# Kernel tuning notes

Hardware: AMD Instinct MI355X
Metric: run time of the kernel (lower is better)

The kernel has to match this reference:

```python
import jax, jax.numpy as jnp
import numpy as np

N_NODES, N_EDGES, N_GRAPHS = 65536, 131072, 2048
F_NODE, F_EDGE, DIM, DIM1, DIM2 = 78, 10, 256, 512, 256
FP_DIM, FP2, FP3, NCB = 1489, 128, 256, 2

PNAMES = []
for _l in (1, 2, 3):
    PNAMES += [f"e{_l}w", f"e{_l}b", f"n{_l}w1", f"n{_l}b1", f"n{_l}w2", f"n{_l}b2",
               f"bn{_l}g", f"bn{_l}b", f"bn{_l}m", f"bn{_l}v"]
PNAMES += ["fcg_w", "fcg_b", "fp1_w", "fp1_b", "fp2_w", "fp2_b",
           "fb1_w", "fb1_b", "fb2_w", "fb2_b", "fb3_w", "fb3_b", "fb4_w", "fb4_b"]


def _params(key):
    ks = iter(jax.random.split(key, 64))
    def rn(*s):
        return jax.random.normal(next(ks), s, dtype=jnp.float32) * 0.05
    def ru(*s):
        return jax.random.uniform(next(ks), s, dtype=jnp.float32)
    p = {}
    for l, ci in zip((1, 2, 3), (F_NODE, DIM1, DIM1)):
        h = DIM if l == 1 else DIM1
        p[f"e{l}w"] = rn(ci, F_EDGE); p[f"e{l}b"] = rn(ci)          # GINEConv edge lin: 10 -> in_channels
        p[f"n{l}w1"] = rn(h, ci);     p[f"n{l}b1"] = rn(h)
        p[f"n{l}w2"] = rn(DIM1, h);   p[f"n{l}b2"] = rn(DIM1)
        p[f"bn{l}g"] = ru(DIM1) + 0.5; p[f"bn{l}b"] = rn(DIM1)
        p[f"bn{l}m"] = rn(DIM1);       p[f"bn{l}v"] = ru(DIM1) + 0.5
    p["fcg_w"] = rn(DIM2, DIM1);  p["fcg_b"] = rn(DIM2)
    p["fp1_w"] = rn(FP2, FP_DIM); p["fp1_b"] = rn(FP2)
    p["fp2_w"] = rn(FP3, FP2);    p["fp2_b"] = rn(FP3)
    for i, (o, ci) in enumerate([(256, 512), (128, 256), (64, 128), (NCB, 64)], 1):
        p[f"fb{i}_w"] = rn(o, ci); p[f"fb{i}_b"] = rn(o)
    return p


def setup_inputs() -> dict:
    key = jax.random.key(0)
    k = jax.random.split(key, 6)
    inp = {
        "x": jax.random.normal(k[0], (N_NODES, F_NODE), dtype=jnp.float32),
        "finger": jax.random.uniform(k[1], (N_GRAPHS, FP_DIM), dtype=jnp.float32),
        "edge_attr": jax.random.normal(k[2], (N_EDGES, F_EDGE), dtype=jnp.float32),
        "edge_index": jax.random.randint(k[3], (2, N_EDGES), 0, N_NODES),
        "batch": jnp.sort(jax.random.randint(k[4], (N_NODES,), 0, N_GRAPHS)),
    }
    inp.update(_params(k[5]))
    return inp


def _lin(x, w, b):
    return x @ w.T + b


def _bn(x, g, b, m, v):
    # eval-mode BatchNorm1d with running stats
    return (x - m) * jax.lax.rsqrt(v + 1e-5) * g + b


def _forward(x, finger, edge_attr, edge_index, batch, p):
    src, dst = edge_index[0], edge_index[1]
    h = x
    for l in (1, 2, 3):
        # GINEConv (eps=0): out = nn(x + sum_j relu(x_j + lin(edge_attr)))
        e = _lin(edge_attr, p[f"e{l}w"], p[f"e{l}b"])               # [E, Cin]
        m = jax.nn.relu(h[src] + e)                                   # gather + edge add
        agg = jax.ops.segment_sum(m, dst, num_segments=N_NODES)      # scatter-add
        t = h + agg
        t = _lin(jax.nn.relu(_lin(t, p[f"n{l}w1"], p[f"n{l}b1"])), p[f"n{l}w2"], p[f"n{l}b2"])
        h = _bn(jax.nn.relu(t), p[f"bn{l}g"], p[f"bn{l}b"], p[f"bn{l}m"], p[f"bn{l}v"])
    g = jax.ops.segment_sum(h, batch, num_segments=N_GRAPHS)         # global_add_pool
    g = jax.nn.relu(_lin(g, p["fcg_w"], p["fcg_b"]))                 # fc_1 (dropout is eval no-op)
    fp = jax.nn.relu(_lin(finger, p["fp1_w"], p["fp1_b"]))
    fp = jax.nn.relu(_lin(fp, p["fp2_w"], p["fp2_b"]))
    y = jnp.concatenate([g, fp], axis=1)                              # [B, 512]
    for i in (1, 2, 3):
        y = jax.nn.relu(_lin(y, p[f"fb{i}_w"], p[f"fb{i}_b"]))
    y = _lin(y, p["fb4_w"], p["fb4_b"])
    return jax.nn.sigmoid(y)


def reference(x, finger, edge_attr, edge_index, batch,
              e1w, e1b, n1w1, n1b1, n1w2, n1b2, bn1g, bn1b, bn1m, bn1v,
              e2w, e2b, n2w1, n2b1, n2w2, n2b2, bn2g, bn2b, bn2m, bn2v,
              e3w, e3b, n3w1, n3b1, n3w2, n3b2, bn3g, bn3b, bn3m, bn3v,
              fcg_w, fcg_b, fp1_w, fp1_b, fp2_w, fp2_b,
              fb1_w, fb1_b, fb2_w, fb2_b, fb3_w, fb3_b, fb4_w, fb4_b):
    args = dict(locals())
    p = {k: args[k] for k in PNAMES}
    return _forward(x, finger, edge_attr, edge_index, batch, p)
```

## Files before the change

### kernel.cpp

```cpp
#include <hip/hip_runtime.h>
#include <stdint.h>

typedef unsigned short u16;
typedef unsigned int u32;
typedef __bf16 bf16x8 __attribute__((ext_vector_type(8)));
typedef float f32x4 __attribute__((ext_vector_type(4)));

#define N_NODES 65536
#define N_EDGES 131072
#define N_GRAPHS 2048

static __device__ __forceinline__ float bf2f(u16 u) {
  union { u32 u; float f; } v; v.u = ((u32)u) << 16; return v.f;
}
static __device__ __forceinline__ u16 f2bf(float f) {
  union { float f; u32 u; } v; v.f = f;
  u32 r = v.u + 0x7fffu + ((v.u >> 16) & 1u);
  return (u16)(r >> 16);
}
static __device__ __forceinline__ void gl16(const void* g, void* l) {
  __builtin_amdgcn_global_load_lds(
      (__attribute__((address_space(1))) void*)(g),
      (__attribute__((address_space(3))) void*)(l), 16, 0, 0);
}

template <int EPI>
__global__ __launch_bounds__(256) void gemm_bt64(
    const u16* __restrict__ A, const u16* __restrict__ W,
    const float* __restrict__ bias, const float* __restrict__ scale,
    const float* __restrict__ shift, u16* __restrict__ Cp,
    int K, int ldc) {
  __shared__ u16 As[128 * 64];
  __shared__ u16 Bs[128 * 64];
  const u32 gx = gridDim.x;
  const u32 nwg = gx * gridDim.y;
  u32 lid = blockIdx.y * gx + blockIdx.x;
  if ((nwg & 7u) == 0u) {
    const u32 cpx = nwg >> 3;
    lid = (lid & 7u) * cpx + (lid >> 3);
  }
  const int bm = (int)(lid / gx) * 128;
  const int bn = (int)(lid % gx) * 128;
  const int tid = threadIdx.x;
  const int lane = tid & 63;
  const int wid = tid >> 6;
  const int wr = wid >> 1, wc = wid & 1;
  const int lg = lane >> 4, lr = lane & 15;

  f32x4 acc[4][4];
#pragma unroll
  for (int i = 0; i < 4; ++i)
#pragma unroll
    for (int j = 0; j < 4; ++j) acc[i][j] = (f32x4){0.f, 0.f, 0.f, 0.f};

  const int srow8 = tid >> 3;
  const int gslot = ((tid & 7) ^ (srow8 & 7)) * 8;
  const u16* Ag[4];
  const u16* Wg[4];
#pragma unroll
  for (int p = 0; p < 4; ++p) {
    Ag[p] = A + (size_t)(bm + p * 32 + srow8) * K + gslot;
    Wg[p] = W + (size_t)(bn + p * 32 + srow8) * K + gslot;
  }
  u16* dA = &As[tid * 8];
  u16* dB = &Bs[tid * 8];

  for (int k0 = 0; k0 < K; k0 += 64) {
#pragma unroll
    for (int p = 0; p < 4; ++p) {
      gl16(Ag[p] + k0, dA + p * 2048);
      gl16(Wg[p] + k0, dB + p * 2048);
    }
    __syncthreads();
#pragma unroll
    for (int kk = 0; kk < 2; ++kk) {
      const int slot = ((kk * 4 + lg) ^ (lr & 7)) * 8;
      bf16x8 af[4], bfv[4];
#pragma unroll
      for (int i = 0; i < 4; ++i)
        af[i] = *(const bf16x8*)&As[(wr * 64 + i * 16 + lr) * 64 + slot];
#pragma unroll
      for (int j = 0; j < 4; ++j)
        bfv[j] = *(const bf16x8*)&Bs[(wc * 64 + j * 16 + lr) * 64 + slot];
#pragma unroll
      for (int i = 0; i < 4; ++i)
#pragma unroll
        for (int j = 0; j < 4; ++j)
          acc[i][j] = __builtin_amdgcn_mfma_f32_16x16x32_bf16(
              af[i], bfv[j], acc[i][j], 0, 0, 0);
    }
    __syncthreads();
  }

#pragma unroll
  for (int i = 0; i < 4; ++i) {
#pragma unroll
    for (int j = 0; j < 4; ++j) {
#pragma unroll
      for (int r = 0; r < 4; ++r) {
        const int grow = bm + wr * 64 + i * 16 + lg * 4 + r;
        const int gcol = bn + wc * 64 + j * 16 + lr;
        float v = acc[i][j][r] + bias[gcol];
        v = fmaxf(v, 0.f);
        if (EPI == 1) v = v * scale[gcol] + shift[gcol];
        Cp[(size_t)grow * ldc + gcol] = f2bf(v);
      }
    }
  }
}

template <int EPI>
__global__ __launch_bounds__(256) void gemm_bt(
    const u16* __restrict__ A, const u16* __restrict__ W,
    const float* __restrict__ bias, const float* __restrict__ scale,
    const float* __restrict__ shift, u16* __restrict__ Cp,
    int K, int ldc, int coff) {
  __shared__ u16 As[128 * 32];
  __shared__ u16 Bs[128 * 32];
  const u32 gx = gridDim.x;
  const u32 nwg = gx * gridDim.y;
  u32 lid = blockIdx.y * gx + blockIdx.x;
  if ((nwg & 7u) == 0u) {
    const u32 cpx = nwg >> 3;
    lid = (lid & 7u) * cpx + (lid >> 3);
  }
  const int bm = (int)(lid / gx) * 128;
  const int bn = (int)(lid % gx) * 128;
  const int tid = threadIdx.x;
  const int lane = tid & 63;
  const int wid = tid >> 6;
  const int wr = wid >> 1, wc = wid & 1;
  const int lg = lane >> 4, lr = lane & 15;

  f32x4 acc[4][4];
#pragma unroll
  for (int i = 0; i < 4; ++i)
#pragma unroll
    for (int j = 0; j < 4; ++j) acc[i][j] = (f32x4){0.f, 0.f, 0.f, 0.f};

  const int srow = tid >> 2;
  const int c8 = (tid & 3) * 8;
  const u16* Ag0 = A + (size_t)(bm + srow) * K + c8;
  const u16* Ag1 = A + (size_t)(bm + 64 + srow) * K + c8;
  const u16* Wg0 = W + (size_t)(bn + srow) * K + c8;
  const u16* Wg1 = W + (size_t)(bn + 64 + srow) * K + c8;
  u16* lA0 = &As[tid * 8];
  u16* lA1 = &As[2048 + tid * 8];
  u16* lB0 = &Bs[tid * 8];
  u16* lB1 = &Bs[2048 + tid * 8];

  for (int k0 = 0; k0 < K; k0 += 32) {
    gl16(Ag0 + k0, lA0);
    gl16(Ag1 + k0, lA1);
    gl16(Wg0 + k0, lB0);
    gl16(Wg1 + k0, lB1);
    __syncthreads();
    bf16x8 af[4], bfv[4];
#pragma unroll
    for (int i = 0; i < 4; ++i)
      af[i] = *(const bf16x8*)&As[(wr * 64 + i * 16 + lr) * 32 + lg * 8];
#pragma unroll
    for (int j = 0; j < 4; ++j)
      bfv[j] = *(const bf16x8*)&Bs[(wc * 64 + j * 16 + lr) * 32 + lg * 8];
#pragma unroll
    for (int i = 0; i < 4; ++i)
#pragma unroll
      for (int j = 0; j < 4; ++j)
        acc[i][j] = __builtin_amdgcn_mfma_f32_16x16x32_bf16(af[i], bfv[j],
                                                            acc[i][j], 0, 0, 0);
    __syncthreads();
  }

#pragma unroll
  for (int i = 0; i < 4; ++i) {
#pragma unroll
    for (int j = 0; j < 4; ++j) {
#pragma unroll
      for (int r = 0; r < 4; ++r) {
        const int grow = bm + wr * 64 + i * 16 + lg * 4 + r;
        const int gcol = bn + wc * 64 + j * 16 + lr;
        float v = acc[i][j][r] + bias[gcol];
        v = fmaxf(v, 0.f);
        if (EPI == 1) v = v * scale[gcol] + shift[gcol];
        Cp[(size_t)grow * ldc + coff + gcol] = f2bf(v);
      }
    }
  }
}

__global__ void hist_deg(const int* __restrict__ dst, int* __restrict__ deg) {
  int e = blockIdx.x * blockDim.x + threadIdx.x;
  if (e < N_EDGES) atomicAdd(&deg[dst[e]], 1);
}

__global__ __launch_bounds__(1024) void scan_rowptr(const int* __restrict__ deg,
                                                    int* __restrict__ rowptr) {
  __shared__ int lds[1024];
  const int t = threadIdx.x;
  const int base = t * 64;
  int s = 0;
  for (int i = 0; i < 64; ++i) s += deg[base + i];
  lds[t] = s;
  __syncthreads();
  for (int ofs = 1; ofs < 1024; ofs <<= 1) {
    int v = (t >= ofs) ? lds[t - ofs] : 0;
    __syncthreads();
    lds[t] += v;
    __syncthreads();
  }
  int run = (t == 0) ? 0 : lds[t - 1];
  for (int i = 0; i < 64; ++i) {
    rowptr[base + i] = run;
    run += deg[base + i];
  }
  if (t == 1023) rowptr[65536] = run;
}

__global__ void scatter_csr(const int* __restrict__ dst,
                            const int* __restrict__ rowptr,
                            int* __restrict__ deg, int* __restrict__ csr) {
  int e = blockIdx.x * blockDim.x + threadIdx.x;
  if (e >= N_EDGES) return;
  int d = dst[e];
  int pos = atomicSub(&deg[d], 1) - 1;
  csr[rowptr[d] + pos] = e;
}

__global__ __launch_bounds__(128) void gather512(
    const int* __restrict__ rowptr, const int* __restrict__ csr,
    const int* __restrict__ esrc, const float* __restrict__ ea,
    const float* __restrict__ ew, const float* __restrict__ eb,
    const u16* __restrict__ H, u16* __restrict__ T) {
  const int t = threadIdx.x;
  const int c4 = t * 4;
  float w[4][10];
#pragma unroll
  for (int j = 0; j < 4; ++j)
#pragma unroll
    for (int k = 0; k < 10; ++k) w[j][k] = ew[(c4 + j) * 10 + k];
  float eb4[4];
#pragma unroll
  for (int j = 0; j < 4; ++j) eb4[j] = eb[c4 + j];

  const int dend = blockIdx.x * 8 + 8;
  for (int d = blockIdx.x * 8; d < dend; ++d) {
    uint2 hv = *(const uint2*)&H[(size_t)d * 512 + c4];
    float a0 = bf2f((u16)(hv.x & 0xffffu)), a1 = bf2f((u16)(hv.x >> 16));
    float a2 = bf2f((u16)(hv.y & 0xffffu)), a3 = bf2f((u16)(hv.y >> 16));
    const int i1 = rowptr[d + 1];
    for (int i = rowptr[d]; i < i1; ++i) {
      const int eid = csr[i];
      const int s = esrc[eid];
      const float2* eap = (const float2*)(ea + (size_t)eid * 10);
      float2 p0 = eap[0], p1 = eap[1], p2 = eap[2], p3 = eap[3], p4 = eap[4];
      const float ev[10] = {p0.x, p0.y, p1.x, p1.y, p2.x,
                            p2.y, p3.x, p3.y, p4.x, p4.y};
      uint2 hs = *(const uint2*)&H[(size_t)s * 512 + c4];
      float h0 = bf2f((u16)(hs.x & 0xffffu)), h1 = bf2f((u16)(hs.x >> 16));
      float h2 = bf2f((u16)(hs.y & 0xffffu)), h3 = bf2f((u16)(hs.y >> 16));
      float e0 = eb4[0], e1 = eb4[1], e2 = eb4[2], e3 = eb4[3];
#pragma unroll
      for (int k = 0; k < 10; ++k) {
        e0 += ev[k] * w[0][k];
        e1 += ev[k] * w[1][k];
        e2 += ev[k] * w[2][k];
        e3 += ev[k] * w[3][k];
      }
      a0 += fmaxf(h0 + e0, 0.f);
      a1 += fmaxf(h1 + e1, 0.f);
      a2 += fmaxf(h2 + e2, 0.f);
      a3 += fmaxf(h3 + e3, 0.f);
    }
    uint2 r;
    r.x = (u32)f2bf(a0) | ((u32)f2bf(a1) << 16);
    r.y = (u32)f2bf(a2) | ((u32)f2bf(a3) << 16);
    *(uint2*)&T[(size_t)d * 512 + c4] = r;
  }
}

__global__ __launch_bounds__(128) void gather78(
    const int* __restrict__ rowptr, const int* __restrict__ csr,
    const int* __restrict__ esrc, const float* __restrict__ ea,
    const float* __restrict__ ew, const float* __restrict__ eb,
    const float* __restrict__ X, u16* __restrict__ T) {
  const int t = threadIdx.x;
  const bool act = t < 78;
  float w[10];
  float ebv = 0.f;
  if (act) {
#pragma unroll
    for (int k = 0; k < 10; ++k) w[k] = ew[t * 10 + k];
    ebv = eb[t];
  }
  const int dend = blockIdx.x * 8 + 8;
  for (int d = blockIdx.x * 8; d < dend; ++d) {
    float acc = act ? X[(size_t)d * 78 + t] : 0.f;
    const int i1 = rowptr[d + 1];
    for (int i = rowptr[d]; i < i1; ++i) {
      const int eid = csr[i];
      const int s = esrc[eid];
      const float2* eap = (const float2*)(ea + (size_t)eid * 10);
      float2 p0 = eap[0], p1 = eap[1], p2 = eap[2], p3 = eap[3], p4 = eap[4];
      const float ev[10] = {p0.x, p0.y, p1.x, p1.y, p2.x,
                            p2.y, p3.x, p3.y, p4.x, p4.y};
      if (act) {
        float el = ebv;
#pragma unroll
        for (int k = 0; k < 10; ++k) el += ev[k] * w[k];
        acc += fmaxf(X[(size_t)s * 78 + t] + el, 0.f);
      }
    }
    if (t < 96) T[(size_t)d * 96 + t] = act ? f2bf(acc) : (u16)0;
  }
}

struct CvtJob { const float* in; u16* out; int cin; int cout; };
struct CvtJobs { CvtJob j[11]; int blk_ofs[12]; };

__global__ __launch_bounds__(256) void cvt_multi(CvtJobs jb, int njobs) {
  int b = blockIdx.x;
  int ji = 0;
  while (ji + 1 < njobs && b >= jb.blk_ofs[ji + 1]) ++ji;
  const CvtJob J = jb.j[ji];
  int idx = (b - jb.blk_ofs[ji]) * 256 + threadIdx.x;
  int r = idx / J.cout, c = idx - r * J.cout;
  int tot_blocks = jb.blk_ofs[ji + 1] - jb.blk_ofs[ji];
  if (idx >= tot_blocks * 256) return;
  if (idx >= ((tot_blocks * 256) / J.cout) * J.cout && c >= J.cout) return;
  J.out[idx] = (c < J.cin) ? f2bf(J.in[(size_t)r * J.cin + c]) : (u16)0;
}

struct BnJobs { const float* g[3]; const float* b[3]; const float* m[3];
                const float* v[3]; };
__global__ void bn_affine3(BnJobs p, float* __restrict__ bnS) {
  int i = blockIdx.x * blockDim.x + threadIdx.x;
  int l = i >> 9, c = i & 511;
  float s = p.g[l][c] * rsqrtf(p.v[l][c] + 1e-5f);
  bnS[l * 1024 + c] = s;
  bnS[l * 1024 + 512 + c] = p.b[l][c] - p.m[l][c] * s;
}

__global__ void seg_starts(const int* __restrict__ batch, int* __restrict__ start,
                           int n, int ngraphs) {
  int i = blockIdx.x * blockDim.x + threadIdx.x;
  if (i >= n) return;
  int b = batch[i];
  int prev = (i == 0) ? -1 : batch[i - 1];
  for (int g = prev + 1; g <= b; ++g) start[g] = i;
  if (i == n - 1)
    for (int g = b + 1; g <= ngraphs; ++g) start[g] = n;
}

__global__ void cvt_pad(const float* __restrict__ in, u16* __restrict__ out,
                        int rows, int cin, int cout) {
  int idx = blockIdx.x * blockDim.x + threadIdx.x;
  if (idx >= rows * cout) return;
  int rrow = idx / cout, j = idx - rrow * cout;
  out[idx] = (j < cin) ? f2bf(in[(size_t)rrow * cin + j]) : (u16)0;
}

__global__ void pool_sum(const u16* __restrict__ H, const int* __restrict__ start,
                         u16* __restrict__ g) {
  int gi = blockIdx.x, c = threadIdx.x;
  int s = start[gi], e = start[gi + 1];
  float acc = 0.f;
  for (int i = s; i < e; ++i) acc += bf2f(H[(size_t)i * 512 + c]);
  g[gi * 512 + c] = f2bf(acc);
}

__global__ void fb34(const u16* __restrict__ y2, const float* __restrict__ w3,
                     const float* __restrict__ b3, const float* __restrict__ w4,
                     const float* __restrict__ b4, float* __restrict__ out) {
  __shared__ float yr[128];
  __shared__ float h3[64];
  const int row = blockIdx.x, t = threadIdx.x;
  yr[t] = bf2f(y2[row * 128 + t]);
  yr[t + 64] = bf2f(y2[row * 128 + 64 + t]);
  __syncthreads();
  float s = b3[t];
  const float* w3r = &w3[t * 128];
#pragma unroll 8
  for (int k = 0; k < 128; ++k) s += yr[k] * w3r[k];
  h3[t] = fmaxf(s, 0.f);
  __syncthreads();
  if (t < 2) {
    float s4 = b4[t];
    const float* w4r = &w4[t * 64];
    for (int k = 0; k < 64; ++k) s4 += h3[k] * w4r[k];
    out[row * 2 + t] = 1.f / (1.f + expf(-s4));
  }
}

#define CDIV(a, b) (((a) + (b)-1) / (b))

extern "C" void kernel_launch(void* const* d_in, const int* in_sizes, int n_in,
                              void* d_out, int out_size, void* d_ws, size_t ws_size,
                              hipStream_t stream) {
  const float* x = (const float*)d_in[0];
  const float* finger = (const float*)d_in[1];
  const float* ea = (const float*)d_in[2];
  const int* eidx = (const int*)d_in[3];
  const int* batch = (const int*)d_in[4];
  const int* esrc = eidx;
  const int* edst = eidx + N_EDGES;

  const float* P[49];
  for (int i = 5; i < 49; ++i) P[i] = (const float*)d_in[i];
  const float* fcg_w = P[35]; const float* fcg_b = P[36];
  const float* fp1_w = P[37]; const float* fp1_b = P[38];
  const float* fp2_w = P[39]; const float* fp2_b = P[40];
  const float* fb1_w = P[41]; const float* fb1_b = P[42];
  const float* fb2_w = P[43]; const float* fb2_b = P[44];
  const float* fb3_w = P[45]; const float* fb3_b = P[46];
  const float* fb4_w = P[47]; const float* fb4_b = P[48];

  size_t off = 0;
  char* base = (char*)d_ws;
  auto alloc = [&](size_t bytes) -> void* {
    void* p = base + off;
    off = (off + bytes + 255) & ~(size_t)255;
    return p;
  };
  char* BA = (char*)alloc((size_t)N_NODES * 512 * 2);
  char* BB = (char*)alloc((size_t)N_NODES * 512 * 2);
  u16* w11 = (u16*)alloc(256 * 96 * 2);
  u16* w12 = (u16*)alloc(512 * 256 * 2);
  u16* w21 = (u16*)alloc(512 * 512 * 2);
  u16* w22 = (u16*)alloc(512 * 512 * 2);
  u16* w31 = (u16*)alloc(512 * 512 * 2);
  u16* w32 = (u16*)alloc(512 * 512 * 2);
  u16* wfcg = (u16*)alloc(256 * 512 * 2);
  u16* wfp1 = (u16*)alloc(128 * 1504 * 2);
  u16* wfp2 = (u16*)alloc(256 * 128 * 2);
  u16* wfb1 = (u16*)alloc(256 * 512 * 2);
  u16* wfb2 = (u16*)alloc(128 * 256 * 2);
  float* bnS = (float*)alloc(6 * 512 * 4);
  int* start = (int*)alloc(2049 * 4);
  int* deg = (int*)alloc(65536 * 4);
  int* rowptr = (int*)alloc(65537 * 4);
  int* csr = (int*)alloc(131072 * 4);
  if (off > ws_size) return;

  u16* fingb = (u16*)BA;
  u16* gbuf = (u16*)(BA + 6160384);
  u16* y0 = (u16*)(BA + 8257536);
  u16* fpa = (u16*)(BA + 10354688);
  u16* y1 = (u16*)(BA + 10878976);
  u16* y2 = (u16*)(BA + 11927552);

  {
    CvtJobs jb;
    const float* ins[11] = {P[5 + 2], P[5 + 4], P[15 + 2], P[15 + 4], P[25 + 2],
                            P[25 + 4], fcg_w, fp1_w, fp2_w, fb1_w, fb2_w};
    u16* outs[11] = {w11, w12, w21, w22, w31, w32, wfcg, wfp1, wfp2, wfb1, wfb2};
    int rows[11] = {256, 512, 512, 512, 512, 512, 256, 128, 256, 256, 128};
    int cins[11] = {78, 256, 512, 512, 512, 512, 512, 1489, 128, 512, 256};
    int couts[11] = {96, 256, 512, 512, 512, 512, 512, 1504, 128, 512, 256};
    int acc = 0;
    for (int i = 0; i < 11; ++i) {
      jb.j[i].in = ins[i]; jb.j[i].out = outs[i];
      jb.j[i].cin = cins[i]; jb.j[i].cout = couts[i];
      jb.blk_ofs[i] = acc;
      acc += CDIV(rows[i] * couts[i], 256);
    }
    jb.blk_ofs[11] = acc;
    cvt_multi<<<acc, 256, 0, stream>>>(jb, 11);
  }
  {
    BnJobs bj;
    for (int l = 0; l < 3; ++l) {
      int pb = 5 + 10 * l;
      bj.g[l] = P[pb + 6]; bj.b[l] = P[pb + 7];
      bj.m[l] = P[pb + 8]; bj.v[l] = P[pb + 9];
    }
    bn_affine3<<<6, 256, 0, stream>>>(bj, bnS);
  }
  seg_starts<<<CDIV(N_NODES, 256), 256, 0, stream>>>(batch, start, N_NODES, N_GRAPHS);

  hipMemsetAsync(deg, 0, 65536 * 4, stream);
  hist_deg<<<CDIV(N_EDGES, 256), 256, 0, stream>>>(edst, deg);
  scan_rowptr<<<1, 1024, 0, stream>>>(deg, rowptr);
  scatter_csr<<<CDIV(N_EDGES, 256), 256, 0, stream>>>(edst, rowptr, deg, csr);

  gather78<<<N_NODES / 8, 128, 0, stream>>>(rowptr, csr, esrc, ea, P[5], P[6], x,
                                            (u16*)BB);
  gemm_bt<0><<<dim3(2, 512), 256, 0, stream>>>((u16*)BB, w11, P[5 + 3], nullptr,
                                               nullptr, (u16*)BA, 96, 256, 0);
  gemm_bt64<1><<<dim3(4, 512), 256, 0, stream>>>((u16*)BA, w12, P[5 + 5], bnS,
                                                 bnS + 512, (u16*)BB, 256, 512);

  gather512<<<N_NODES / 8, 128, 0, stream>>>(rowptr, csr, esrc, ea, P[15], P[16],
                                             (const u16*)BB, (u16*)BA);
  gemm_bt64<0><<<dim3(4, 512), 256, 0, stream>>>((u16*)BA, w21, P[15 + 3], nullptr,
                                                 nullptr, (u16*)BB, 512, 512);
  gemm_bt64<1><<<dim3(4, 512), 256, 0, stream>>>((u16*)BB, w22, P[15 + 5],
                                                 bnS + 1024, bnS + 1024 + 512,
                                                 (u16*)BA, 512, 512);

  gather512<<<N_NODES / 8, 128, 0, stream>>>(rowptr, csr, esrc, ea, P[25], P[26],
                                             (const u16*)BA, (u16*)BB);
  gemm_bt64<0><<<dim3(4, 512), 256, 0, stream>>>((u16*)BB, w31, P[25 + 3], nullptr,
                                                 nullptr, (u16*)BA, 512, 512);
  gemm_bt64<1><<<dim3(4, 512), 256, 0, stream>>>((u16*)BA, w32, P[25 + 5],
                                                 bnS + 2048, bnS + 2048 + 512,
                                                 (u16*)BB, 512, 512);

  pool_sum<<<N_GRAPHS, 512, 0, stream>>>((const u16*)BB, start, gbuf);
  cvt_pad<<<CDIV(N_GRAPHS * 1504, 256), 256, 0, stream>>>(finger, fingb, N_GRAPHS,
                                                          1489, 1504);
  gemm_bt<0><<<dim3(2, 16), 256, 0, stream>>>(gbuf, wfcg, fcg_b, nullptr, nullptr,
                                              y0, 512, 512, 0);
  gemm_bt<0><<<dim3(1, 16), 256, 0, stream>>>(fingb, wfp1, fp1_b, nullptr, nullptr,
                                              fpa, 1504, 128, 0);
  gemm_bt<0><<<dim3(2, 16), 256, 0, stream>>>(fpa, wfp2, fp2_b, nullptr, nullptr,
                                              y0, 128, 512, 256);
  gemm_bt<0><<<dim3(2, 16), 256, 0, stream>>>(y0, wfb1, fb1_b, nullptr, nullptr,
                                              y1, 512, 256, 0);
  gemm_bt<0><<<dim3(1, 16), 256, 0, stream>>>(y1, wfb2, fb2_b, nullptr, nullptr,
                                              y2, 256, 128, 0);
  fb34<<<N_GRAPHS, 64, 0, stream>>>(y2, fb3_w, fb3_b, fb4_w, fb4_b, (float*)d_out);
}
```

Measured before the change: 588.3 us.

## Pre-sort edge data into CSR order and use fp16 dot2 for edge linear

Adds a prep pass that gathers edge sources and edge attributes into CSR order, packing the attributes as fp16 pairs, so the layer-2/3 gathers read edges contiguously instead of going through csr->eid indirection. The per-edge 10-wide edge linear now uses packed fp16 dot2 instructions with fp16-converted weights, cutting the FMA count. The inner loop is also unrolled by two. The cost is an extra prep kernel, extra workspace, and reduced precision from fp16 edge attributes and weights.

```diff
diff --git a/kernel.cpp b/kernel.cpp
--- a/kernel.cpp
+++ b/kernel.cpp
@@ -5,6 +5,7 @@
 typedef unsigned int u32;
 typedef __bf16 bf16x8 __attribute__((ext_vector_type(8)));
 typedef float f32x4 __attribute__((ext_vector_type(4)));
+typedef _Float16 h2 __attribute__((ext_vector_type(2)));
 
 #define N_NODES 65536
 #define N_EDGES 131072
@@ -23,6 +24,19 @@
       (__attribute__((address_space(1))) void*)(g),
       (__attribute__((address_space(3))) void*)(l), 16, 0, 0);
 }
+static __device__ __forceinline__ h2 b2h2(u32 u) {
+  union { u32 u; h2 h; } v; v.u = u; return v.h;
+}
+static __device__ __forceinline__ u32 pk2h(float a, float b) {
+  union { _Float16 h[2]; u32 u; } v;
+  v.h[0] = (_Float16)a; v.h[1] = (_Float16)b; return v.u;
+}
+#if __has_builtin(__builtin_amdgcn_fdot2)
+#define FDOT2(a, b, c) __builtin_amdgcn_fdot2((a), (b), (c), false)
+#else
+#define FDOT2(a, b, c) \
+  ((c) + (float)(a)[0] * (float)(b)[0] + (float)(a)[1] * (float)(b)[1])
+#endif
 
 template <int EPI>
 __global__ __launch_bounds__(256) void gemm_bt64(
@@ -226,18 +240,46 @@
   csr[rowptr[d] + pos] = e;
 }
 
-__global__ __launch_bounds__(128) void gather512(
-    const int* __restrict__ rowptr, const int* __restrict__ csr,
-    const int* __restrict__ esrc, const float* __restrict__ ea,
-    const float* __restrict__ ew, const float* __restrict__ eb,
-    const u16* __restrict__ H, u16* __restrict__ T) {
+__global__ void prep_edges(const int* __restrict__ csr,
+                           const int* __restrict__ esrc,
+                           const float* __restrict__ ea,
+                           int* __restrict__ src_s, u32* __restrict__ ea16) {
+  int i = blockIdx.x * blockDim.x + threadIdx.x;
+  if (i >= N_EDGES) return;
+  const int eid = csr[i];
+  src_s[i] = esrc[eid];
+  const float* er = ea + (size_t)eid * 10;
+  u32* o = ea16 + (size_t)i * 5;
+  o[0] = pk2h(er[0], er[1]);
+  o[1] = pk2h(er[2], er[3]);
+  o[2] = pk2h(er[4], er[5]);
+  o[3] = pk2h(er[6], er[7]);
+  o[4] = pk2h(er[8], er[9]);
+}
+
+__global__ void ew_h16(const float* __restrict__ ew2,
+                       const float* __restrict__ ew3, u32* __restrict__ o2,
+                       u32* __restrict__ o3) {
+  int i = blockIdx.x * blockDim.x + threadIdx.x;
+  if (i >= 1024) return;
+  const float* src = (i < 512) ? ew2 + (size_t)i * 10 : ew3 + (size_t)(i - 512) * 10;
+  u32* dst = (i < 512) ? o2 + i * 5 : o3 + (i - 512) * 5;
+#pragma unroll
+  for (int k = 0; k < 5; ++k) dst[k] = pk2h(src[2 * k], src[2 * k + 1]);
+}
+
+__global__ __launch_bounds__(128) void gather512d(
+    const int* __restrict__ rowptr, const int* __restrict__ src_s,
+    const u32* __restrict__ ea16, const u32* __restrict__ ew16,
+    const float* __restrict__ eb, const u16* __restrict__ H,
+    u16* __restrict__ T) {
   const int t = threadIdx.x;
   const int c4 = t * 4;
-  float w[4][10];
+  h2 w[4][5];
 #pragma unroll
   for (int j = 0; j < 4; ++j)
 #pragma unroll
-    for (int k = 0; k < 10; ++k) w[j][k] = ew[(c4 + j) * 10 + k];
+    for (int k = 0; k < 5; ++k) w[j][k] = b2h2(ew16[(c4 + j) * 5 + k]);
   float eb4[4];
 #pragma unroll
   for (int j = 0; j < 4; ++j) eb4[j] = eb[c4 + j];
@@ -248,28 +290,32 @@
     float a0 = bf2f((u16)(hv.x & 0xffffu)), a1 = bf2f((u16)(hv.x >> 16));
     float a2 = bf2f((u16)(hv.y & 0xffffu)), a3 = bf2f((u16)(hv.y >> 16));
     const int i1 = rowptr[d + 1];
+#pragma unroll 2
     for (int i = rowptr[d]; i < i1; ++i) {
-      const int eid = csr[i];
-      const int s = esrc[eid];
-      const float2* eap = (const float2*)(ea + (size_t)eid * 10);
-      float2 p0 = eap[0], p1 = eap[1], p2 = eap[2], p3 = eap[3], p4 = eap[4];
-      const float ev[10] = {p0.x, p0.y, p1.x, p1.y, p2.x,
-                            p2.y, p3.x, p3.y, p4.x, p4.y};
+      const int s = src_s[i];
+      const u32* ep = ea16 + (size_t)i * 5;
+      const h2 e0 = b2h2(ep[0]), e1 = b2h2(ep[1]), e2 = b2h2(ep[2]),
+               e3 = b2h2(ep[3]), e4 = b2h2(ep[4]);
       uint2 hs = *(const uint2*)&H[(size_t)s * 512 + c4];
       float h0 = bf2f((u16)(hs.x & 0xffffu)), h1 = bf2f((u16)(hs.x >> 16));
-      float h2 = bf2f((u16)(hs.y & 0xffffu)), h3 = bf2f((u16)(hs.y >> 16));
-      float e0 = eb4[0], e1 = eb4[1], e2 = eb4[2], e3 = eb4[3];
-#pragma unroll
-      for (int k = 0; k < 10; ++k) {
-        e0 += ev[k] * w[0][k];
-        e1 += ev[k] * w[1][k];
-        e2 += ev[k] * w[2][k];
-        e3 += ev[k] * w[3][k];
-      }
-      a0 += fmaxf(h0 + e0, 0.f);
-      a1 += fmaxf(h1 + e1, 0.f);
-      a2 += fmaxf(h2 + e2, 0.f);
-      a3 += fmaxf(h3 + e3, 0.f);
+      float h2v = bf2f((u16)(hs.y & 0xffffu)), h3 = bf2f((u16)(hs.y >> 16));
+      float l0 = eb4[0], l1 = eb4[1], l2 = eb4[2], l3 = eb4[3];
+      l0 = FDOT2(e0, w[0][0], l0); l0 = FDOT2(e1, w[0][1], l0);
+      l0 = FDOT2(e2, w[0][2], l0); l0 = FDOT2(e3, w[0][3], l0);
+      l0 = FDOT2(e4, w[0][4], l0);
+      l1 = FDOT2(e0, w[1][0], l1); l1 = FDOT2(e1, w[1][1], l1);
+      l1 = FDOT2(e2, w[1][2], l1); l1 = FDOT2(e3, w[1][3], l1);
+      l1 = FDOT2(e4, w[1][4], l1);
+      l2 = FDOT2(e0, w[2][0], l2); l2 = FDOT2(e1, w[2][1], l2);
+      l2 = FDOT2(e2, w[2][2], l2); l2 = FDOT2(e3, w[2][3], l2);
+      l2 = FDOT2(e4, w[2][4], l2);
+      l3 = FDOT2(e0, w[3][0], l3); l3 = FDOT2(e1, w[3][1], l3);
+      l3 = FDOT2(e2, w[3][2], l3); l3 = FDOT2(e3, w[3][3], l3);
+      l3 = FDOT2(e4, w[3][4], l3);
+      a0 += fmaxf(h0 + l0, 0.f);
+      a1 += fmaxf(h1 + l1, 0.f);
+      a2 += fmaxf(h2v + l2, 0.f);
+      a3 += fmaxf(h3 + l3, 0.f);
     }
     uint2 r;
     r.x = (u32)f2bf(a0) | ((u32)f2bf(a1) << 16);
@@ -439,6 +485,10 @@
   int* deg = (int*)alloc(65536 * 4);
   int* rowptr = (int*)alloc(65537 * 4);
   int* csr = (int*)alloc(131072 * 4);
+  int* src_s = (int*)alloc(131072 * 4);
+  u32* ea16 = (u32*)alloc((size_t)131072 * 5 * 4);
+  u32* ew16a = (u32*)alloc(512 * 5 * 4);
+  u32* ew16b = (u32*)alloc(512 * 5 * 4);
   if (off > ws_size) return;
 
   u16* fingb = (u16*)BA;
@@ -476,11 +526,13 @@
     bn_affine3<<<6, 256, 0, stream>>>(bj, bnS);
   }
   seg_starts<<<CDIV(N_NODES, 256), 256, 0, stream>>>(batch, start, N_NODES, N_GRAPHS);
+  ew_h16<<<4, 256, 0, stream>>>(P[15], P[25], ew16a, ew16b);
 
   hipMemsetAsync(deg, 0, 65536 * 4, stream);
   hist_deg<<<CDIV(N_EDGES, 256), 256, 0, stream>>>(edst, deg);
   scan_rowptr<<<1, 1024, 0, stream>>>(deg, rowptr);
   scatter_csr<<<CDIV(N_EDGES, 256), 256, 0, stream>>>(edst, rowptr, deg, csr);
+  prep_edges<<<CDIV(N_EDGES, 256), 256, 0, stream>>>(csr, esrc, ea, src_s, ea16);
 
   gather78<<<N_NODES / 8, 128, 0, stream>>>(rowptr, csr, esrc, ea, P[5], P[6], x,
                                             (u16*)BB);
@@ -489,16 +541,16 @@
   gemm_bt64<1><<<dim3(4, 512), 256, 0, stream>>>((u16*)BA, w12, P[5 + 5], bnS,
                                                  bnS + 512, (u16*)BB, 256, 512);
 
-  gather512<<<N_NODES / 8, 128, 0, stream>>>(rowptr, csr, esrc, ea, P[15], P[16],
-                                             (const u16*)BB, (u16*)BA);
+  gather512d<<<N_NODES / 8, 128, 0, stream>>>(rowptr, src_s, ea16, ew16a, P[16],
+                                              (const u16*)BB, (u16*)BA);
   gemm_bt64<0><<<dim3(4, 512), 256, 0, stream>>>((u16*)BA, w21, P[15 + 3], nullptr,
                                                  nullptr, (u16*)BB, 512, 512);
   gemm_bt64<1><<<dim3(4, 512), 256, 0, stream>>>((u16*)BB, w22, P[15 + 5],
                                                  bnS + 1024, bnS + 1024 + 512,
                                                  (u16*)BA, 512, 512);
 
-  gather512<<<N_NODES / 8, 128, 0, stream>>>(rowptr, csr, esrc, ea, P[25], P[26],
-                                             (const u16*)BA, (u16*)BB);
+  gather512d<<<N_NODES / 8, 128, 0, stream>>>(rowptr, src_s, ea16, ew16b, P[26],
+                                              (const u16*)BA, (u16*)BB);
   gemm_bt64<0><<<dim3(4, 512), 256, 0, stream>>>((u16*)BB, w31, P[25 + 3], nullptr,
                                                  nullptr, (u16*)BA, 512, 512);
   gemm_bt64<1><<<dim3(4, 512), 256, 0, stream>>>((u16*)BA, w32, P[25 + 5],
```

Result: faster. 566.6 us (-3.7%).
